# Optimization experiments

Hardware: AMD Instinct MI355X
Metric: run time of the kernel (lower is better)

## Reference

```python
import jax, jax.numpy as jnp
import numpy as np

BS, G, L, D = 64, 64, 100, 64


def setup_inputs() -> dict:
    key = jax.random.key(0)
    ks = jax.random.split(key, 12)
    s = 1.0 / np.sqrt(D)
    return {
        "seqs": jax.random.normal(ks[0], (BS, G, L, D), dtype=jnp.float32),
        "lens": jax.random.randint(ks[1], (BS, G, 1), 1, L + 1, dtype=jnp.int32),
        "W1": jax.random.normal(ks[2], (D, D), dtype=jnp.float32) * s,
        "W2": jax.random.normal(ks[3], (D, D), dtype=jnp.float32) * s,
        "W3": jax.random.normal(ks[4], (D, D), dtype=jnp.float32) * s,
        "b": jnp.zeros((D,), dtype=jnp.float32),
        "p": jax.random.normal(ks[5], (D,), dtype=jnp.float32) * s,
        "Wq": jax.random.normal(ks[6], (D, 2 * D), dtype=jnp.float32) * s,
        "Wl_0": jax.random.normal(ks[7], (2 * D, 2 * D), dtype=jnp.float32) * s,
        "bl_0": jnp.zeros((2 * D,), dtype=jnp.float32),
        "Wl_1": jax.random.normal(ks[8], (2 * D, 2 * D), dtype=jnp.float32) * s,
        "bl_1": jnp.zeros((2 * D,), dtype=jnp.float32),
    }


def reference(seqs, lens, W1, W2, W3, b, p, Wq, Wl_0, bl_0, Wl_1, bl_1):
    # seqs: [bs, g, L, d]; lens: [bs, g, 1]
    V_last = jnp.einsum('bgd,de->bge', seqs[:, :, -1, :], W1)[:, :, None, :]
    V_seq = jnp.einsum('bgld,de->bgle', seqs, W2)
    avg = jnp.sum(seqs, axis=-2) / lens.astype(jnp.float32)  # [bs, g, d]
    V_avg = jnp.einsum('bgd,de->bge', avg, W3)[:, :, None, :]
    emb = jnp.einsum('bgld,d->bgl', V_last + V_seq + V_avg + b, p)  # [bs, g, L]
    attn = jax.nn.softmax(emb, axis=-1)
    weighted = jnp.einsum('bgl,bgld->bgd', attn, seqs)  # attention-weighted pooling
    h0 = weighted @ Wq  # [bs, g, 2d]
    h = jax.nn.relu(h0 @ Wl_0 + bl_0)
    h = jax.nn.relu(h @ Wl_1 + bl_1)
    return h0 + h  # residual
```

## Files before the change

kernel.cpp:

```cpp
#include <hip/hip_runtime.h>
#include <cstddef>

#define LL 100
#define DD 64
#define NG 4

template<int CTRL>
__device__ __forceinline__ float dpp_add(float x) {
    int s = __builtin_amdgcn_update_dpp(0, __float_as_int(x), CTRL, 0xF, 0xF, true);
    return x + __int_as_float(s);
}

__device__ __forceinline__ float sum16_all(float x) {
    x = dpp_add<0xB1>(x);
    x = dpp_add<0x4E>(x);
    x = dpp_add<0x141>(x);
    x = dpp_add<0x140>(x);
    return x;
}

__global__ __launch_bounds__(256, 4) void seq_encoder_fused(
    const float* __restrict__ seqs,
    const float* __restrict__ W2,  const float* __restrict__ p,
    const float* __restrict__ Wq,  const float* __restrict__ Wl0,
    const float* __restrict__ bl0, const float* __restrict__ Wl1,
    const float* __restrict__ bl1, float* __restrict__ out)
{
    __shared__ __align__(16) float s_q2[DD];
    __shared__ __align__(16) float s_w[NG][DD];
    __shared__ __align__(16) float s_p[2][NG][2 * DD];
    __shared__ __align__(16) float s_h0[NG][2 * DD];
    __shared__ __align__(16) float s_h1[NG][2 * DD];

    const int tid = threadIdx.x;
    const int r = tid >> 6;
    const int lane = tid & 63;

    {
        const int row = tid >> 2, part = tid & 3;
        const float* wrow = W2 + row * DD + part * 16;
        const float* pp = p + part * 16;
        float s = 0.f;
        #pragma unroll
        for (int e = 0; e < 16; ++e) s += wrow[e] * pp[e];
        s += __shfl_down(s, 2);
        s += __shfl_down(s, 1);
        if (part == 0) s_q2[row] = s;
    }
    __syncthreads();

    const int rg = lane >> 4;
    const int cb = lane & 15;
    const float4 q2v = *(const float4*)&s_q2[cb * 4];

    const int gi = blockIdx.x * NG + r;
    const float4* Sp = (const float4*)(seqs + (size_t)gi * (LL * DD)) + (rg * 16 + cb);

    float z = 0.f;
    float wx = 0.f, wy = 0.f, wz = 0.f, ww = 0.f;

    float4 buf[2][5];
    #pragma unroll
    for (int j = 0; j < 5; ++j) buf[0][j] = Sp[j * 64];
    #pragma unroll
    for (int b = 0; b < 5; ++b) {
        if (b < 4) {
            #pragma unroll
            for (int j = 0; j < 5; ++j)
                buf[(b + 1) & 1][j] = Sp[((b + 1) * 5 + j) * 64];
        }
        #pragma unroll
        for (int j = 0; j < 5; ++j) {
            float4 x = buf[b & 1][j];
            float t = x.x * q2v.x + x.y * q2v.y + x.z * q2v.z + x.w * q2v.w;
            t = sum16_all(t);
            float e = __expf(t);
            z += e;
            wx += e * x.x;
            wy += e * x.y;
            wz += e * x.z;
            ww += e * x.w;
        }
    }

    z  += __shfl_xor(z, 16);  z  += __shfl_xor(z, 32);
    wx += __shfl_xor(wx, 16); wx += __shfl_xor(wx, 32);
    wy += __shfl_xor(wy, 16); wy += __shfl_xor(wy, 32);
    wz += __shfl_xor(wz, 16); wz += __shfl_xor(wz, 32);
    ww += __shfl_xor(ww, 16); ww += __shfl_xor(ww, 32);

    const float invz = 1.f / z;
    if (rg == 0) {
        float4 o;
        o.x = wx * invz; o.y = wy * invz; o.z = wz * invz; o.w = ww * invz;
        *(float4*)&s_w[r][cb * 4] = o;
    }
    __syncthreads();

    const int jt = tid & 127;
    const int hf = tid >> 7;
    const int g0 = 2 * hf;

    {
        float p0 = 0.f, p1 = 0.f, p2 = 0.f, p3 = 0.f;
        const int k0 = hf * 32;
        for (int k = k0; k < k0 + 32; ++k) {
            float wv = Wq[k * (2 * DD) + jt];
            p0 += s_w[0][k] * wv;
            p1 += s_w[1][k] * wv;
            p2 += s_w[2][k] * wv;
            p3 += s_w[3][k] * wv;
        }
        s_p[hf][0][jt] = p0; s_p[hf][1][jt] = p1;
        s_p[hf][2][jt] = p2; s_p[hf][3][jt] = p3;
    }
    __syncthreads();
    {
        float ha = s_p[0][g0][jt] + s_p[1][g0][jt];
        float hb = s_p[0][g0 + 1][jt] + s_p[1][g0 + 1][jt];
        s_h0[g0][jt] = ha;
        s_h0[g0 + 1][jt] = hb;
    }
    __syncthreads();

    {
        float p0 = 0.f, p1 = 0.f, p2 = 0.f, p3 = 0.f;
        const int k0 = hf * 64;
        for (int k = k0; k < k0 + 64; ++k) {
            float wv = Wl0[k * (2 * DD) + jt];
            p0 += s_h0[0][k] * wv;
            p1 += s_h0[1][k] * wv;
            p2 += s_h0[2][k] * wv;
            p3 += s_h0[3][k] * wv;
        }
        s_p[hf][0][jt] = p0; s_p[hf][1][jt] = p1;
        s_p[hf][2][jt] = p2; s_p[hf][3][jt] = p3;
    }
    __syncthreads();
    {
        float bv = bl0[jt];
        float ha = fmaxf(s_p[0][g0][jt] + s_p[1][g0][jt] + bv, 0.f);
        float hb = fmaxf(s_p[0][g0 + 1][jt] + s_p[1][g0 + 1][jt] + bv, 0.f);
        s_h1[g0][jt] = ha;
        s_h1[g0 + 1][jt] = hb;
    }
    __syncthreads();

    {
        float p0 = 0.f, p1 = 0.f, p2 = 0.f, p3 = 0.f;
        const int k0 = hf * 64;
        for (int k = k0; k < k0 + 64; ++k) {
            float wv = Wl1[k * (2 * DD) + jt];
            p0 += s_h1[0][k] * wv;
            p1 += s_h1[1][k] * wv;
            p2 += s_h1[2][k] * wv;
            p3 += s_h1[3][k] * wv;
        }
        s_p[hf][0][jt] = p0; s_p[hf][1][jt] = p1;
        s_p[hf][2][jt] = p2; s_p[hf][3][jt] = p3;
    }
    __syncthreads();
    {
        float bv = bl1[jt];
        float oa = fmaxf(s_p[0][g0][jt] + s_p[1][g0][jt] + bv, 0.f);
        float ob = fmaxf(s_p[0][g0 + 1][jt] + s_p[1][g0 + 1][jt] + bv, 0.f);
        const size_t gbase = (size_t)blockIdx.x * NG;
        out[(gbase + g0) * (2 * DD) + jt]     = s_h0[g0][jt] + oa;
        out[(gbase + g0 + 1) * (2 * DD) + jt] = s_h0[g0 + 1][jt] + ob;
    }
}

extern "C" void kernel_launch(void* const* d_in, const int* in_sizes, int n_in,
                              void* d_out, int out_size, void* d_ws, size_t ws_size,
                              hipStream_t stream) {
    const float* seqs = (const float*)d_in[0];
    const float* W2   = (const float*)d_in[3];
    const float* p    = (const float*)d_in[6];
    const float* Wq   = (const float*)d_in[7];
    const float* Wl0  = (const float*)d_in[8];
    const float* bl0  = (const float*)d_in[9];
    const float* Wl1  = (const float*)d_in[10];
    const float* bl1  = (const float*)d_in[11];
    float* out = (float*)d_out;

    const int n_groups = 64 * 64;
    seq_encoder_fused<<<n_groups / NG, 256, 0, stream>>>(
        seqs, W2, p, Wq, Wl0, bl0, Wl1, bl1, out);
}
```

Measured before the change: 180.5 us.

## Split each group's sequence across two waves and double block size

Doubles the block to 512 threads so each group's 100-row sequence is split between two wavefronts (13 and 12 row-chunks each). Their partial softmax sums are combined through shared memory. The downstream MLP matmuls are split four ways along K instead of two. The aim is more memory-level parallelism and shorter per-wave serial chains in the streaming phase, at the cost of an extra shared-memory reduction and barrier, a smaller prefetch buffer, and tighter register limits from the launch bounds.

```diff
diff --git a/kernel.cpp b/kernel.cpp
--- a/kernel.cpp
+++ b/kernel.cpp
@@ -19,7 +19,37 @@
     return x;
 }
 
-__global__ __launch_bounds__(256, 4) void seq_encoder_fused(
+template<int NP>
+__device__ __forceinline__ void attn_pass(const float4* __restrict__ Sp, const float4 q2v,
+                                          float& z, float& wx, float& wy, float& wzv, float& ww) {
+    constexpr int B = 3;
+    constexpr int NB = (NP + B - 1) / B;
+    float4 buf[2][B];
+    #pragma unroll
+    for (int j = 0; j < B; ++j) buf[0][j] = Sp[j * 64];
+    #pragma unroll
+    for (int b = 0; b < NB; ++b) {
+        #pragma unroll
+        for (int j = 0; j < B; ++j) {
+            const int idx = (b + 1) * B + j;
+            if (idx < NP) buf[(b + 1) & 1][j] = Sp[idx * 64];
+        }
+        #pragma unroll
+        for (int j = 0; j < B; ++j) {
+            const int idx = b * B + j;
+            if (idx < NP) {
+                float4 x = buf[b & 1][j];
+                float t = x.x * q2v.x + x.y * q2v.y + x.z * q2v.z + x.w * q2v.w;
+                t = sum16_all(t);
+                float e = __expf(t);
+                z += e;
+                wx += e * x.x; wy += e * x.y; wzv += e * x.z; ww += e * x.w;
+            }
+        }
+    }
+}
+
+__global__ __launch_bounds__(512, 8) void seq_encoder_fused(
     const float* __restrict__ seqs,
     const float* __restrict__ W2,  const float* __restrict__ p,
     const float* __restrict__ Wq,  const float* __restrict__ Wl0,
@@ -27,22 +57,25 @@
     const float* __restrict__ bl1, float* __restrict__ out)
 {
     __shared__ __align__(16) float s_q2[DD];
+    __shared__ __align__(16) float s_wp[8][DD];
+    __shared__ float s_zp[8];
     __shared__ __align__(16) float s_w[NG][DD];
-    __shared__ __align__(16) float s_p[2][NG][2 * DD];
+    __shared__ __align__(16) float s_p[4][NG][2 * DD];
     __shared__ __align__(16) float s_h0[NG][2 * DD];
     __shared__ __align__(16) float s_h1[NG][2 * DD];
 
     const int tid = threadIdx.x;
-    const int r = tid >> 6;
+    const int w = tid >> 6;
     const int lane = tid & 63;
 
     {
-        const int row = tid >> 2, part = tid & 3;
-        const float* wrow = W2 + row * DD + part * 16;
-        const float* pp = p + part * 16;
+        const int row = tid >> 3, part = tid & 7;
+        const float* wrow = W2 + row * DD + part * 8;
+        const float* pp = p + part * 8;
         float s = 0.f;
         #pragma unroll
-        for (int e = 0; e < 16; ++e) s += wrow[e] * pp[e];
+        for (int e = 0; e < 8; ++e) s += wrow[e] * pp[e];
+        s += __shfl_down(s, 4);
         s += __shfl_down(s, 2);
         s += __shfl_down(s, 1);
         if (part == 0) s_q2[row] = s;
@@ -53,120 +86,86 @@
     const int cb = lane & 15;
     const float4 q2v = *(const float4*)&s_q2[cb * 4];
 
-    const int gi = blockIdx.x * NG + r;
-    const float4* Sp = (const float4*)(seqs + (size_t)gi * (LL * DD)) + (rg * 16 + cb);
+    const int g  = w >> 1;
+    const int hf = w & 1;
+    const int gi = blockIdx.x * NG + g;
+    const float4* Sp = (const float4*)(seqs + (size_t)gi * (LL * DD))
+                       + (rg * 16 + cb) + (hf ? 13 * 64 : 0);
 
-    float z = 0.f;
-    float wx = 0.f, wy = 0.f, wz = 0.f, ww = 0.f;
+    float z = 0.f, wx = 0.f, wy = 0.f, wzv = 0.f, ww = 0.f;
+    if (hf == 0) attn_pass<13>(Sp, q2v, z, wx, wy, wzv, ww);
+    else         attn_pass<12>(Sp, q2v, z, wx, wy, wzv, ww);
 
-    float4 buf[2][5];
-    #pragma unroll
-    for (int j = 0; j < 5; ++j) buf[0][j] = Sp[j * 64];
-    #pragma unroll
-    for (int b = 0; b < 5; ++b) {
-        if (b < 4) {
-            #pragma unroll
-            for (int j = 0; j < 5; ++j)
-                buf[(b + 1) & 1][j] = Sp[((b + 1) * 5 + j) * 64];
-        }
-        #pragma unroll
-        for (int j = 0; j < 5; ++j) {
-            float4 x = buf[b & 1][j];
-            float t = x.x * q2v.x + x.y * q2v.y + x.z * q2v.z + x.w * q2v.w;
-            t = sum16_all(t);
-            float e = __expf(t);
-            z += e;
-            wx += e * x.x;
-            wy += e * x.y;
-            wz += e * x.z;
-            ww += e * x.w;
-        }
+    z   += __shfl_xor(z, 16);   z   += __shfl_xor(z, 32);
+    wx  += __shfl_xor(wx, 16);  wx  += __shfl_xor(wx, 32);
+    wy  += __shfl_xor(wy, 16);  wy  += __shfl_xor(wy, 32);
+    wzv += __shfl_xor(wzv, 16); wzv += __shfl_xor(wzv, 32);
+    ww  += __shfl_xor(ww, 16);  ww  += __shfl_xor(ww, 32);
+
+    if (rg == 0) {
+        float4 o; o.x = wx; o.y = wy; o.z = wzv; o.w = ww;
+        *(float4*)&s_wp[w][cb * 4] = o;
     }
+    if (lane == 0) s_zp[w] = z;
+    __syncthreads();
 
-    z  += __shfl_xor(z, 16);  z  += __shfl_xor(z, 32);
-    wx += __shfl_xor(wx, 16); wx += __shfl_xor(wx, 32);
-    wy += __shfl_xor(wy, 16); wy += __shfl_xor(wy, 32);
-    wz += __shfl_xor(wz, 16); wz += __shfl_xor(wz, 32);
-    ww += __shfl_xor(ww, 16); ww += __shfl_xor(ww, 32);
-
-    const float invz = 1.f / z;
-    if (rg == 0) {
-        float4 o;
-        o.x = wx * invz; o.y = wy * invz; o.z = wz * invz; o.w = ww * invz;
-        *(float4*)&s_w[r][cb * 4] = o;
+    if (tid < NG * DD) {
+        const int g2 = tid >> 6, k = tid & 63;
+        const float invz = 1.f / (s_zp[2 * g2] + s_zp[2 * g2 + 1]);
+        s_w[g2][k] = (s_wp[2 * g2][k] + s_wp[2 * g2 + 1][k]) * invz;
     }
     __syncthreads();
 
     const int jt = tid & 127;
-    const int hf = tid >> 7;
-    const int g0 = 2 * hf;
+    const int q  = tid >> 7;
 
     {
         float p0 = 0.f, p1 = 0.f, p2 = 0.f, p3 = 0.f;
-        const int k0 = hf * 32;
-        for (int k = k0; k < k0 + 32; ++k) {
+        const int k0 = q * 16;
+        for (int k = k0; k < k0 + 16; ++k) {
             float wv = Wq[k * (2 * DD) + jt];
-            p0 += s_w[0][k] * wv;
-            p1 += s_w[1][k] * wv;
-            p2 += s_w[2][k] * wv;
-            p3 += s_w[3][k] * wv;
+            p0 += s_w[0][k] * wv; p1 += s_w[1][k] * wv;
+            p2 += s_w[2][k] * wv; p3 += s_w[3][k] * wv;
         }
-        s_p[hf][0][jt] = p0; s_p[hf][1][jt] = p1;
-        s_p[hf][2][jt] = p2; s_p[hf][3][jt] = p3;
+        s_p[q][0][jt] = p0; s_p[q][1][jt] = p1;
+        s_p[q][2][jt] = p2; s_p[q][3][jt] = p3;
     }
     __syncthreads();
-    {
-        float ha = s_p[0][g0][jt] + s_p[1][g0][jt];
-        float hb = s_p[0][g0 + 1][jt] + s_p[1][g0 + 1][jt];
-        s_h0[g0][jt] = ha;
-        s_h0[g0 + 1][jt] = hb;
-    }
+    s_h0[q][jt] = s_p[0][q][jt] + s_p[1][q][jt] + s_p[2][q][jt] + s_p[3][q][jt];
     __syncthreads();
 
     {
         float p0 = 0.f, p1 = 0.f, p2 = 0.f, p3 = 0.f;
-        const int k0 = hf * 64;
-        for (int k = k0; k < k0 + 64; ++k) {
+        const int k0 = q * 32;
+        for (int k = k0; k < k0 + 32; ++k) {
             float wv = Wl0[k * (2 * DD) + jt];
-            p0 += s_h0[0][k] * wv;
-            p1 += s_h0[1][k] * wv;
-            p2 += s_h0[2][k] * wv;
-            p3 += s_h0[3][k] * wv;
+            p0 += s_h0[0][k] * wv; p1 += s_h0[1][k] * wv;
+            p2 += s_h0[2][k] * wv; p3 += s_h0[3][k] * wv;
         }
-        s_p[hf][0][jt] = p0; s_p[hf][1][jt] = p1;
-        s_p[hf][2][jt] = p2; s_p[hf][3][jt] = p3;
+        s_p[q][0][jt] = p0; s_p[q][1][jt] = p1;
+        s_p[q][2][jt] = p2; s_p[q][3][jt] = p3;
     }
     __syncthreads();
-    {
-        float bv = bl0[jt];
-        float ha = fmaxf(s_p[0][g0][jt] + s_p[1][g0][jt] + bv, 0.f);
-        float hb = fmaxf(s_p[0][g0 + 1][jt] + s_p[1][g0 + 1][jt] + bv, 0.f);
-        s_h1[g0][jt] = ha;
-        s_h1[g0 + 1][jt] = hb;
-    }
+    s_h1[q][jt] = fmaxf(s_p[0][q][jt] + s_p[1][q][jt] + s_p[2][q][jt] + s_p[3][q][jt]
+                        + bl0[jt], 0.f);
     __syncthreads();
 
     {
         float p0 = 0.f, p1 = 0.f, p2 = 0.f, p3 = 0.f;
-        const int k0 = hf * 64;
-        for (int k = k0; k < k0 + 64; ++k) {
+        const int k0 = q * 32;
+        for (int k = k0; k < k0 + 32; ++k) {
             float wv = Wl1[k * (2 * DD) + jt];
-            p0 += s_h1[0][k] * wv;
-            p1 += s_h1[1][k] * wv;
-            p2 += s_h1[2][k] * wv;
-            p3 += s_h1[3][k] * wv;
+            p0 += s_h1[0][k] * wv; p1 += s_h1[1][k] * wv;
+            p2 += s_h1[2][k] * wv; p3 += s_h1[3][k] * wv;
         }
-        s_p[hf][0][jt] = p0; s_p[hf][1][jt] = p1;
-        s_p[hf][2][jt] = p2; s_p[hf][3][jt] = p3;
+        s_p[q][0][jt] = p0; s_p[q][1][jt] = p1;
+        s_p[q][2][jt] = p2; s_p[q][3][jt] = p3;
     }
     __syncthreads();
     {
-        float bv = bl1[jt];
-        float oa = fmaxf(s_p[0][g0][jt] + s_p[1][g0][jt] + bv, 0.f);
-        float ob = fmaxf(s_p[0][g0 + 1][jt] + s_p[1][g0 + 1][jt] + bv, 0.f);
-        const size_t gbase = (size_t)blockIdx.x * NG;
-        out[(gbase + g0) * (2 * DD) + jt]     = s_h0[g0][jt] + oa;
-        out[(gbase + g0 + 1) * (2 * DD) + jt] = s_h0[g0 + 1][jt] + ob;
+        float o = fmaxf(s_p[0][q][jt] + s_p[1][q][jt] + s_p[2][q][jt] + s_p[3][q][jt]
+                        + bl1[jt], 0.f);
+        out[((size_t)blockIdx.x * NG + q) * (2 * DD) + jt] = s_h0[q][jt] + o;
     }
 }
 
@@ -184,6 +183,6 @@
     float* out = (float*)d_out;
 
     const int n_groups = 64 * 64;
-    seq_encoder_fused<<<n_groups / NG, 256, 0, stream>>>(
+    seq_encoder_fused<<<n_groups / NG, 512, 0, stream>>>(
         seqs, W2, p, Wq, Wl0, bl0, Wl1, bl1, out);
 }
```

Measured after the change: 196.4 us. +8.8%, slower.
